# Kernel optimization log

Hardware: AMD Instinct MI355X
Metric: run time of the kernel (lower is better)

Reference implementation:

```python
import jax, jax.numpy as jnp
import numpy as np

B, N, IN_DIM = 2, 2048, 1024
DIM, DEPTH, HEADS, DH = 512, 4, 8, 128
INNER = HEADS * DH  # 1024
MLP, NCLS = 1024, 2
EPS = 1e-5


def setup_inputs() -> dict:
    key = jax.random.key(0)
    ks = jax.random.split(key, 10)
    r = lambda k, shape: (jax.random.normal(k, shape, dtype=jnp.float32) * 0.02)
    return {
        "x": jax.random.normal(ks[0], (B, N, IN_DIM), dtype=jnp.float32),
        "mask": jnp.ones((B, N), dtype=jnp.float32),
        "proj_w": r(ks[1], (IN_DIM, DIM)),
        "proj_b": jnp.zeros((DIM,), jnp.float32),
        "cls_token": jax.random.normal(ks[2], (1, 1, DIM), dtype=jnp.float32),
        "ln1_g": jnp.ones((DEPTH, DIM), jnp.float32),
        "ln1_b": jnp.zeros((DEPTH, DIM), jnp.float32),
        "qkv_w": r(ks[3], (DEPTH, DIM, 3 * INNER)),
        "out_w": r(ks[4], (DEPTH, INNER, DIM)),
        "out_b": jnp.zeros((DEPTH, DIM), jnp.float32),
        "ln2_g": jnp.ones((DEPTH, DIM), jnp.float32),
        "ln2_b": jnp.zeros((DEPTH, DIM), jnp.float32),
        "ff_w1": r(ks[5], (DEPTH, DIM, MLP)),
        "ff_b1": jnp.zeros((DEPTH, MLP), jnp.float32),
        "ff_w2": r(ks[6], (DEPTH, MLP, DIM)),
        "ff_b2": jnp.zeros((DEPTH, DIM), jnp.float32),
        "norm_g": jnp.ones((DIM,), jnp.float32),
        "norm_b": jnp.zeros((DIM,), jnp.float32),
        "head_ln_g": jnp.ones((DIM,), jnp.float32),
        "head_ln_b": jnp.zeros((DIM,), jnp.float32),
        "head_w": r(ks[7], (DIM, NCLS)),
        "head_b": jnp.zeros((NCLS,), jnp.float32),
    }


def _ln(x, g, b):
    m = jnp.mean(x, axis=-1, keepdims=True)
    v = jnp.mean((x - m) ** 2, axis=-1, keepdims=True)
    return (x - m) * jax.lax.rsqrt(v + EPS) * g + b


def reference(x, mask, proj_w, proj_b, cls_token, ln1_g, ln1_b, qkv_w, out_w,
              out_b, ln2_g, ln2_b, ff_w1, ff_b1, ff_w2, ff_b2, norm_g, norm_b,
              head_ln_g, head_ln_b, head_w, head_b):
    b = x.shape[0]
    scale = DH ** -0.5
    # input projection + ReLU
    h = jax.nn.relu(x @ proj_w + proj_b)  # [b, n, dim]
    # prepend cls token; extend mask with a 1 for it
    cls = jnp.broadcast_to(cls_token, (b, 1, DIM))
    h = jnp.concatenate([cls, h], axis=1)  # [b, n+1, dim]
    m_full = jnp.concatenate([jnp.ones((b, 1), mask.dtype), mask], axis=1)
    keep = (m_full != 0)[:, None, None, :]  # [b,1,1,n+1]

    for l in range(DEPTH):  # NOTE: original blocks have NO residual connections
        hn = _ln(h, ln1_g[l], ln1_b[l])
        qkv = hn @ qkv_w[l]  # [b, n+1, 3*inner]
        q, k, v = jnp.split(qkv, 3, axis=-1)
        resh = lambda t: t.reshape(b, -1, HEADS, DH).transpose(0, 2, 1, 3)
        q, k, v = resh(q), resh(k), resh(v)  # [b, h, n+1, dh]
        dots = jnp.einsum('bhid,bhjd->bhij', q, k) * scale
        dots = jnp.where(keep, dots, -jnp.inf)
        attn = jax.nn.softmax(dots, axis=-1)
        o = jnp.einsum('bhij,bhjd->bhid', attn, v)
        o = o.transpose(0, 2, 1, 3).reshape(b, -1, INNER)
        h = o @ out_w[l] + out_b[l]  # attention out (no residual)
        hn = _ln(h, ln2_g[l], ln2_b[l])
        h = jax.nn.gelu(hn @ ff_w1[l] + ff_b1[l], approximate=False) @ ff_w2[l] + ff_b2[l]

    pooled = h[:, 0]  # cls pooling
    pooled = _ln(pooled, norm_g, norm_b)
    pooled = _ln(pooled, head_ln_g, head_ln_b)
    return pooled @ head_w + head_b  # [b, num_classes]
```

## Files before the change

### kernel.cpp

```cpp
#include <hip/hip_runtime.h>
#include <hip/hip_bf16.h>
#include <stdint.h>

#define B_      2
#define N_      2048
#define S_      2049
#define SP_     2176
#define MP_     (B_*SP_)
#define IN_DIM_ 1024
#define DIM_    512
#define HEADS_  8
#define DH_     128
#define INNER_  1024
#define MLP_    1024
#define DEPTH_  4
#define NKV_    (SP_/64)
#define NCHUNK_ 4
#define TPC_    9

typedef __bf16 bf16;
typedef __bf16 bf16x4 __attribute__((ext_vector_type(4)));
typedef __bf16 bf16x8 __attribute__((ext_vector_type(8)));
typedef float  f32x4  __attribute__((ext_vector_type(4)));

__device__ __forceinline__ int sw64(int r, int c)  { return r*64  + (c ^ ((r&7)<<3)); }
__device__ __forceinline__ int sw128(int r, int c) { return r*128 + (c ^ ((r&7)<<3)); }
__device__ __forceinline__ int swr64(int r, int c) { return r*64  + (c ^ ((((r&7)^((r>>3)&7)))<<3)); }

__global__ __launch_bounds__(256) void wconv_kernel(const float* __restrict__ src,
                                                    bf16* __restrict__ dst,
                                                    int K, int N)
{
    __shared__ float tile[32][33];
    size_t mo = (size_t)blockIdx.z * K * N;
    int n0 = blockIdx.x * 32, k0 = blockIdx.y * 32;
    int tx = threadIdx.x & 31, ty = threadIdx.x >> 5;
#pragma unroll
    for (int i = 0; i < 32; i += 8)
        tile[ty + i][tx] = src[mo + (size_t)(k0 + ty + i) * N + n0 + tx];
    __syncthreads();
#pragma unroll
    for (int i = 0; i < 32; i += 8)
        dst[mo + (size_t)(n0 + ty + i) * K + k0 + tx] = (bf16)tile[tx][ty + i];
}

__global__ __launch_bounds__(256) void xconv_kernel(const float* __restrict__ x,
                                                    bf16* __restrict__ xb)
{
    int idx = blockIdx.x * 256 + threadIdx.x;
    int row = idx >> 7;
    int c   = (idx & 127) * 8;
    int b = row / SP_, s = row - b * SP_;
    bf16x8 v;
    if (s >= 1 && s <= N_) {
        const float* src = x + (size_t)(b * N_ + s - 1) * IN_DIM_ + c;
#pragma unroll
        for (int i = 0; i < 8; ++i) v[i] = (bf16)src[i];
    } else {
#pragma unroll
        for (int i = 0; i < 8; ++i) v[i] = (bf16)0.f;
    }
    *(bf16x8*)&xb[(size_t)row * IN_DIM_ + c] = v;
}

__global__ __launch_bounds__(256) void mask_kernel(const float* __restrict__ mask,
                                                   float* __restrict__ pb)
{
    int j = blockIdx.x * 256 + threadIdx.x;
    int b = blockIdx.y;
    if (j >= SP_) return;
    float v;
    if (j == 0) v = 0.f;
    else if (j <= N_) v = (mask[(size_t)b * N_ + j - 1] != 0.f) ? 0.f : -1e30f;
    else v = -1e30f;
    pb[(size_t)b * SP_ + j] = v;
}

__global__ void cls_kernel(const float* __restrict__ cls, float* __restrict__ h)
{
    h[(size_t)(blockIdx.x * SP_) * DIM_ + threadIdx.x] = cls[threadIdx.x];
}

__global__ __launch_bounds__(256) void ln_kernel(const float* __restrict__ h,
                                                 const float* __restrict__ g,
                                                 const float* __restrict__ bta,
                                                 bf16* __restrict__ out)
{
    int row  = blockIdx.x * 4 + (threadIdx.x >> 6);
    int lane = threadIdx.x & 63;
    const float* x = h + (size_t)row * DIM_;
    float v[8]; float s = 0.f;
#pragma unroll
    for (int i = 0; i < 8; ++i) { v[i] = x[lane + 64 * i]; s += v[i]; }
#pragma unroll
    for (int o = 32; o; o >>= 1) s += __shfl_xor(s, o);
    float mean = s * (1.f / DIM_);
    float vs = 0.f;
#pragma unroll
    for (int i = 0; i < 8; ++i) { float d = v[i] - mean; vs += d * d; }
#pragma unroll
    for (int o = 32; o; o >>= 1) vs += __shfl_xor(vs, o);
    float rstd = rsqrtf(vs * (1.f / DIM_) + 1e-5f);
    bf16* orow = out + (size_t)row * DIM_;
#pragma unroll
    for (int i = 0; i < 8; ++i)
        orow[lane + 64 * i] = (bf16)((v[i] - mean) * rstd * g[lane + 64 * i] + bta[lane + 64 * i]);
}

template<int BM, int BN, int ACT, int OUTBF>
__global__ __launch_bounds__(256) void gemm_bt(const bf16* __restrict__ A,
                                               const bf16* __restrict__ Bt,
                                               const float* __restrict__ bias,
                                               void* __restrict__ Cp,
                                               int M, int N, int K)
{
    constexpr int MF = (BM == 128) ? 4 : ((BN == 128) ? 4 : 2);
    constexpr int NF = (BM == 128) ? 4 : 2;
    constexpr int AT = BM / 32, BT = BN / 32;
    __shared__ __align__(16) bf16 As[BM * 64];
    __shared__ __align__(16) bf16 Bs[BN * 64];
    const int tid  = threadIdx.x;
    const int wave = tid >> 6, lane = tid & 63;
    const int bm = blockIdx.x * BM, bn = blockIdx.y * BN;
    const int wr = (BM == 128) ? (wave >> 1) * 64 : ((BN == 64) ? (wave >> 1) * 32 : 0);
    const int wc = (BM == 128) ? (wave & 1) * 64 : ((BN == 64) ? (wave & 1) * 32 : wave * 32);
    const int fr = lane & 15, fk = (lane >> 4) * 8;

    f32x4 acc[MF][NF];
#pragma unroll
    for (int m = 0; m < MF; ++m)
#pragma unroll
        for (int n = 0; n < NF; ++n) acc[m][n] = (f32x4){0.f, 0.f, 0.f, 0.f};

    bf16x8 apre[AT], bpre[BT];
    auto ldg = [&](int k0) {
#pragma unroll
        for (int t = 0; t < AT; ++t) {
            int e = (t * 256 + tid) * 8;
            apre[t] = *(const bf16x8*)&A[(size_t)(bm + (e >> 6)) * K + k0 + (e & 63)];
        }
#pragma unroll
        for (int t = 0; t < BT; ++t) {
            int e = (t * 256 + tid) * 8;
            bpre[t] = *(const bf16x8*)&Bt[(size_t)(bn + (e >> 6)) * K + k0 + (e & 63)];
        }
    };

    ldg(0);
    for (int k0 = 0; k0 < K; k0 += 64) {
        __syncthreads();
#pragma unroll
        for (int t = 0; t < AT; ++t) {
            int e = (t * 256 + tid) * 8;
            *(bf16x8*)&As[sw64(e >> 6, e & 63)] = apre[t];
        }
#pragma unroll
        for (int t = 0; t < BT; ++t) {
            int e = (t * 256 + tid) * 8;
            *(bf16x8*)&Bs[sw64(e >> 6, e & 63)] = bpre[t];
        }
        __syncthreads();
        if (k0 + 64 < K) ldg(k0 + 64);
#pragma unroll
        for (int kk = 0; kk < 2; ++kk) {
            bf16x8 af[MF], bb[NF];
#pragma unroll
            for (int m = 0; m < MF; ++m) af[m] = *(const bf16x8*)&As[sw64(wr + m * 16 + fr, kk * 32 + fk)];
#pragma unroll
            for (int n = 0; n < NF; ++n) bb[n] = *(const bf16x8*)&Bs[sw64(wc + n * 16 + fr, kk * 32 + fk)];
#pragma unroll
            for (int m = 0; m < MF; ++m)
#pragma unroll
                for (int n = 0; n < NF; ++n)
                    acc[m][n] = __builtin_amdgcn_mfma_f32_16x16x32_bf16(af[m], bb[n], acc[m][n], 0, 0, 0);
        }
    }

    const int fc = lane & 15, fr4 = (lane >> 4) * 4;
#pragma unroll
    for (int n = 0; n < NF; ++n) {
        int col = bn + wc + n * 16 + fc;
        float bv = bias ? bias[col] : 0.f;
#pragma unroll
        for (int m = 0; m < MF; ++m) {
#pragma unroll
            for (int j = 0; j < 4; ++j) {
                int row = bm + wr + m * 16 + fr4 + j;
                float v = acc[m][n][j] + bv;
                if (ACT == 1) v = fmaxf(v, 0.f);
                if (ACT == 2) v = 0.5f * v * (1.f + erff(v * 0.70710678118654752f));
                if (OUTBF) ((bf16*)Cp)[(size_t)row * N + col] = (bf16)v;
                else       ((float*)Cp)[(size_t)row * N + col] = v;
            }
        }
    }
}

__global__ __launch_bounds__(256) void attn_kernel(const bf16* __restrict__ qkv,
                                                   const float* __restrict__ pb,
                                                   bf16* __restrict__ o0,
                                                   bf16* __restrict__ o1,
                                                   bf16* __restrict__ o2,
                                                   bf16* __restrict__ o3,
                                                   float* __restrict__ mlbuf)
{
    __shared__ __align__(16) bf16 KsPs[64 * 128];
    __shared__ __align__(16) bf16 Vt[128 * 64];
    __shared__ float Msk[64];

    const int bh = blockIdx.x, b = bh >> 3, hh = bh & 7;
    const int q0 = blockIdx.y * 128;
    const int chunk = blockIdx.z;
    const int t0 = chunk * TPC_;
    const int t1 = (t0 + TPC_ < NKV_) ? t0 + TPC_ : NKV_;
    bf16* obuf = (chunk == 0) ? o0 : (chunk == 1) ? o1 : (chunk == 2) ? o2 : o3;

    const int tid = threadIdx.x, wave = tid >> 6, lane = tid & 63;
    const int fc = lane & 15, g = lane >> 4, g8 = g * 8, rr0 = g * 4;
    bf16* Pw = &KsPs[wave * 2048];

    const bf16* qb = qkv + (size_t)(b * SP_) * (3 * INNER_) + hh * DH_;
    const bf16* kb = qb + INNER_;
    const bf16* vb = qb + 2 * INNER_;

    bf16x8 aq[2][4];
#pragma unroll
    for (int m = 0; m < 2; ++m)
#pragma unroll
        for (int kk = 0; kk < 4; ++kk)
            aq[m][kk] = *(const bf16x8*)&qb[(size_t)(q0 + wave * 32 + m * 16 + fc) * (3 * INNER_) + kk * 32 + g8];

    const int srow = tid >> 4;
    const int scol = (tid & 15) * 8;
    bf16x8 kreg[4], vreg[4];
    float mreg;

    f32x4 accO[2][8];
#pragma unroll
    for (int m = 0; m < 2; ++m)
#pragma unroll
        for (int f = 0; f < 8; ++f) accO[m][f] = (f32x4){0.f, 0.f, 0.f, 0.f};
    float mrow[2] = {-3e38f, -3e38f};
    float lrow[2] = {0.f, 0.f};
    const float scale = 0.08838834764831845f;

    auto issue = [&](int kt) {
        int j0 = kt * 64;
#pragma unroll
        for (int t = 0; t < 4; ++t) {
            kreg[t] = *(const bf16x8*)&kb[(size_t)(j0 + t * 16 + srow) * (3 * INNER_) + scol];
            vreg[t] = *(const bf16x8*)&vb[(size_t)(j0 + t * 16 + srow) * (3 * INNER_) + scol];
        }
        mreg = pb[(size_t)b * SP_ + j0 + (tid & 63)];
    };

    issue(t0);
    for (int kt = t0; kt < t1; ++kt) {
        __syncthreads();
        {
#pragma unroll
            for (int t = 0; t < 4; ++t) {
                *(bf16x8*)&KsPs[sw128(t * 16 + srow, scol)] = kreg[t];
#pragma unroll
                for (int i = 0; i < 8; ++i) Vt[swr64(scol + i, t * 16 + srow)] = vreg[t][i];
            }
            if (tid < 64) Msk[tid] = mreg;
        }
        __syncthreads();
        if (kt + 1 < t1) issue(kt + 1);

        f32x4 sf[2][4];
#pragma unroll
        for (int m = 0; m < 2; ++m)
#pragma unroll
            for (int f = 0; f < 4; ++f) sf[m][f] = (f32x4){0.f, 0.f, 0.f, 0.f};
        __builtin_amdgcn_s_setprio(1);
#pragma unroll
        for (int kk = 0; kk < 4; ++kk) {
            bf16x8 bk[4];
#pragma unroll
            for (int f = 0; f < 4; ++f) bk[f] = *(const bf16x8*)&KsPs[sw128(f * 16 + fc, kk * 32 + g8)];
#pragma unroll
            for (int m = 0; m < 2; ++m)
#pragma unroll
                for (int f = 0; f < 4; ++f)
                    sf[m][f] = __builtin_amdgcn_mfma_f32_16x16x32_bf16(bk[f], aq[m][kk], sf[m][f], 0, 0, 0);
        }
        __builtin_amdgcn_s_setprio(0);

        float rmax[2] = {-3e38f, -3e38f};
#pragma unroll
        for (int f = 0; f < 4; ++f) {
            f32x4 mb = *(const f32x4*)&Msk[f * 16 + rr0];
#pragma unroll
            for (int m = 0; m < 2; ++m)
#pragma unroll
                for (int r = 0; r < 4; ++r) {
                    float s = sf[m][f][r] * scale + mb[r];
                    sf[m][f][r] = s;
                    rmax[m] = fmaxf(rmax[m], s);
                }
        }
#pragma unroll
        for (int m = 0; m < 2; ++m) {
            rmax[m] = fmaxf(rmax[m], __shfl_xor(rmax[m], 16));
            rmax[m] = fmaxf(rmax[m], __shfl_xor(rmax[m], 32));
            if (__any(rmax[m] > mrow[m] + 5.f)) {
                float mn = fmaxf(mrow[m], rmax[m]);
                float corr = __expf(mrow[m] - mn);
                mrow[m] = mn;
                lrow[m] *= corr;
                float c0 = __shfl(corr, rr0 + 0);
                float c1 = __shfl(corr, rr0 + 1);
                float c2 = __shfl(corr, rr0 + 2);
                float c3 = __shfl(corr, rr0 + 3);
#pragma unroll
                for (int f = 0; f < 8; ++f) {
                    accO[m][f][0] *= c0; accO[m][f][1] *= c1;
                    accO[m][f][2] *= c2; accO[m][f][3] *= c3;
                }
            }
        }
        bf16x4 pw[2][4];
#pragma unroll
        for (int m = 0; m < 2; ++m)
#pragma unroll
            for (int f = 0; f < 4; ++f) {
#pragma unroll
                for (int r = 0; r < 4; ++r) {
                    float p = __expf(sf[m][f][r] - mrow[m]);
                    lrow[m] += p;
                    pw[m][f][r] = (bf16)p;
                }
            }
        __syncthreads();
#pragma unroll
        for (int m = 0; m < 2; ++m)
#pragma unroll
            for (int f = 0; f < 4; ++f)
                *(bf16x4*)&Pw[swr64(m * 16 + fc, f * 16 + rr0)] = pw[m][f];

        __builtin_amdgcn_s_setprio(1);
#pragma unroll
        for (int kk = 0; kk < 2; ++kk) {
            bf16x8 ap[2];
#pragma unroll
            for (int m = 0; m < 2; ++m) ap[m] = *(const bf16x8*)&Pw[swr64(m * 16 + fc, kk * 32 + g8)];
#pragma unroll
            for (int f = 0; f < 8; ++f) {
                bf16x8 bv = *(const bf16x8*)&Vt[swr64(f * 16 + fc, kk * 32 + g8)];
#pragma unroll
                for (int m = 0; m < 2; ++m)
                    accO[m][f] = __builtin_amdgcn_mfma_f32_16x16x32_bf16(ap[m], bv, accO[m][f], 0, 0, 0);
            }
        }
        __builtin_amdgcn_s_setprio(0);
    }

#pragma unroll
    for (int m = 0; m < 2; ++m) {
        float l = lrow[m];
        l += __shfl_xor(l, 16);
        l += __shfl_xor(l, 32);
        if (g == 0) {
            int q = q0 + wave * 32 + m * 16 + fc;
            size_t mi = ((size_t)(chunk * B_ * HEADS_ + bh) * SP_ + q) * 2;
            mlbuf[mi + 0] = mrow[m];
            mlbuf[mi + 1] = l;
        }
        float linv = (l > 0.f) ? 1.f / l : 0.f;
        float l0 = __shfl(linv, rr0 + 0);
        float l1 = __shfl(linv, rr0 + 1);
        float l2 = __shfl(linv, rr0 + 2);
        float l3 = __shfl(linv, rr0 + 3);
#pragma unroll
        for (int f = 0; f < 8; ++f) {
            int col = hh * DH_ + f * 16 + fc;
            size_t base = (size_t)(b * SP_ + q0 + wave * 32 + m * 16 + rr0) * INNER_ + col;
            obuf[base + 0 * INNER_] = (bf16)(accO[m][f][0] * l0);
            obuf[base + 1 * INNER_] = (bf16)(accO[m][f][1] * l1);
            obuf[base + 2 * INNER_] = (bf16)(accO[m][f][2] * l2);
            obuf[base + 3 * INNER_] = (bf16)(accO[m][f][3] * l3);
        }
    }
}

__global__ __launch_bounds__(256) void attn_combine_kernel(const bf16* __restrict__ o0,
                                                           const bf16* __restrict__ o1,
                                                           const bf16* __restrict__ o2,
                                                           bf16* __restrict__ o3,
                                                           const float* __restrict__ mlbuf)
{
    const int bh = blockIdx.y, b = bh >> 3, hh = bh & 7;
    int gx = blockIdx.x * 256 + threadIdx.x;
    int q  = gx >> 4;
    int d  = (gx & 15) * 8;

    float mv[NCHUNK_], lv[NCHUNK_];
#pragma unroll
    for (int c = 0; c < NCHUNK_; ++c) {
        size_t mi = ((size_t)(c * B_ * HEADS_ + bh) * SP_ + q) * 2;
        mv[c] = mlbuf[mi];
        lv[c] = mlbuf[mi + 1];
    }
    float M = mv[0];
#pragma unroll
    for (int c = 1; c < NCHUNK_; ++c) M = fmaxf(M, mv[c]);
    float w[NCHUNK_], den = 0.f;
#pragma unroll
    for (int c = 0; c < NCHUNK_; ++c) { w[c] = lv[c] * __expf(mv[c] - M); den += w[c]; }
    float r = (den > 0.f) ? 1.f / den : 0.f;

    size_t base = (size_t)(b * SP_ + q) * INNER_ + hh * DH_ + d;
    bf16x8 v0 = *(const bf16x8*)&o0[base];
    bf16x8 v1 = *(const bf16x8*)&o1[base];
    bf16x8 v2 = *(const bf16x8*)&o2[base];
    bf16x8 v3 = *(const bf16x8*)&o3[base];
    bf16x8 out;
#pragma unroll
    for (int i = 0; i < 8; ++i)
        out[i] = (bf16)((w[0] * (float)v0[i] + w[1] * (float)v1[i]
                       + w[2] * (float)v2[i] + w[3] * (float)v3[i]) * r);
    *(bf16x8*)&o3[base] = out;
}

__global__ __launch_bounds__(64) void head_kernel(const float* __restrict__ h,
                                                  const float* __restrict__ ng, const float* __restrict__ nb,
                                                  const float* __restrict__ hg, const float* __restrict__ hb,
                                                  const float* __restrict__ hw, const float* __restrict__ hbi,
                                                  float* __restrict__ out)
{
    int b = blockIdx.x, lane = threadIdx.x;
    const float* xr = h + (size_t)(b * SP_) * DIM_;
    float v[8]; float s = 0.f;
#pragma unroll
    for (int i = 0; i < 8; ++i) { v[i] = xr[lane + 64 * i]; s += v[i]; }
#pragma unroll
    for (int o = 32; o; o >>= 1) s += __shfl_xor(s, o);
    float mean = s * (1.f / DIM_); float vs = 0.f;
#pragma unroll
    for (int i = 0; i < 8; ++i) { float d = v[i] - mean; vs += d * d; }
#pragma unroll
    for (int o = 32; o; o >>= 1) vs += __shfl_xor(vs, o);
    float rstd = rsqrtf(vs * (1.f / DIM_) + 1e-5f);
#pragma unroll
    for (int i = 0; i < 8; ++i) v[i] = (v[i] - mean) * rstd * ng[lane + 64 * i] + nb[lane + 64 * i];
    s = 0.f;
#pragma unroll
    for (int i = 0; i < 8; ++i) s += v[i];
#pragma unroll
    for (int o = 32; o; o >>= 1) s += __shfl_xor(s, o);
    mean = s * (1.f / DIM_); vs = 0.f;
#pragma unroll
    for (int i = 0; i < 8; ++i) { float d = v[i] - mean; vs += d * d; }
#pragma unroll
    for (int o = 32; o; o >>= 1) vs += __shfl_xor(vs, o);
    rstd = rsqrtf(vs * (1.f / DIM_) + 1e-5f);
#pragma unroll
    for (int i = 0; i < 8; ++i) v[i] = (v[i] - mean) * rstd * hg[lane + 64 * i] + hb[lane + 64 * i];
    float a0 = 0.f, a1 = 0.f;
#pragma unroll
    for (int i = 0; i < 8; ++i) {
        a0 += v[i] * hw[(lane + 64 * i) * 2 + 0];
        a1 += v[i] * hw[(lane + 64 * i) * 2 + 1];
    }
#pragma unroll
    for (int o = 32; o; o >>= 1) { a0 += __shfl_xor(a0, o); a1 += __shfl_xor(a1, o); }
    if (lane == 0) { out[b * 2 + 0] = a0 + hbi[0]; out[b * 2 + 1] = a1 + hbi[1]; }
}

extern "C" void kernel_launch(void* const* d_in, const int* in_sizes, int n_in,
                              void* d_out, int out_size, void* d_ws, size_t ws_size,
                              hipStream_t stream)
{
    const float* x       = (const float*)d_in[0];
    const float* mask    = (const float*)d_in[1];
    const float* proj_w  = (const float*)d_in[2];
    const float* proj_b  = (const float*)d_in[3];
    const float* cls_tok = (const float*)d_in[4];
    const float* ln1_g   = (const float*)d_in[5];
    const float* ln1_b   = (const float*)d_in[6];
    const float* qkv_w   = (const float*)d_in[7];
    const float* out_w   = (const float*)d_in[8];
    const float* out_b   = (const float*)d_in[9];
    const float* ln2_g   = (const float*)d_in[10];
    const float* ln2_b   = (const float*)d_in[11];
    const float* ff_w1   = (const float*)d_in[12];
    const float* ff_b1   = (const float*)d_in[13];
    const float* ff_w2   = (const float*)d_in[14];
    const float* ff_b2   = (const float*)d_in[15];
    const float* norm_g  = (const float*)d_in[16];
    const float* norm_b  = (const float*)d_in[17];
    const float* hln_g   = (const float*)d_in[18];
    const float* hln_b   = (const float*)d_in[19];
    const float* head_w  = (const float*)d_in[20];
    const float* head_b  = (const float*)d_in[21];

    char* p = (char*)d_ws;
    auto alloc = [&](size_t bytes) { char* r = p; p += (bytes + 255) & ~(size_t)255; return r; };
    bf16*  x_bf    = (bf16*)alloc((size_t)MP_ * IN_DIM_ * 2);
    float* h       = (float*)alloc((size_t)MP_ * DIM_ * 4);
    bf16*  hn_bf   = (bf16*)alloc((size_t)MP_ * DIM_ * 2);
    bf16*  qkv_bf  = (bf16*)alloc((size_t)MP_ * 3 * INNER_ * 2);
    bf16*  o_bf    = (bf16*)alloc((size_t)MP_ * INNER_ * 2);
    bf16*  ff1_bf  = (bf16*)alloc((size_t)MP_ * MLP_ * 2);
    bf16*  proj_wt = (bf16*)alloc((size_t)DIM_ * IN_DIM_ * 2);
    bf16*  qkv_wt  = (bf16*)alloc((size_t)DEPTH_ * 3 * INNER_ * DIM_ * 2);
    bf16*  out_wt  = (bf16*)alloc((size_t)DEPTH_ * DIM_ * INNER_ * 2);
    bf16*  ff1_wt  = (bf16*)alloc((size_t)DEPTH_ * MLP_ * DIM_ * 2);
    bf16*  ff2_wt  = (bf16*)alloc((size_t)DEPTH_ * DIM_ * MLP_ * 2);
    float* pbias   = (float*)alloc((size_t)B_ * SP_ * 4);
    if ((size_t)(p - (char*)d_ws) > ws_size) return;
    float* mlbuf = (float*)hn_bf;

    wconv_kernel<<<dim3(DIM_ / 32, IN_DIM_ / 32, 1), 256, 0, stream>>>(proj_w, proj_wt, IN_DIM_, DIM_);
    wconv_kernel<<<dim3(3 * INNER_ / 32, DIM_ / 32, DEPTH_), 256, 0, stream>>>(qkv_w, qkv_wt, DIM_, 3 * INNER_);
    wconv_kernel<<<dim3(DIM_ / 32, INNER_ / 32, DEPTH_), 256, 0, stream>>>(out_w, out_wt, INNER_, DIM_);
    wconv_kernel<<<dim3(MLP_ / 32, DIM_ / 32, DEPTH_), 256, 0, stream>>>(ff_w1, ff1_wt, DIM_, MLP_);
    wconv_kernel<<<dim3(DIM_ / 32, MLP_ / 32, DEPTH_), 256, 0, stream>>>(ff_w2, ff2_wt, MLP_, DIM_);

    xconv_kernel<<<MP_ * IN_DIM_ / 8 / 256, 256, 0, stream>>>(x, x_bf);
    mask_kernel<<<dim3((SP_ + 255) / 256, B_), 256, 0, stream>>>(mask, pbias);

    gemm_bt<64, 64, 1, 0><<<dim3(MP_ / 64, DIM_ / 64), 256, 0, stream>>>(x_bf, proj_wt, proj_b, h, MP_, DIM_, IN_DIM_);
    cls_kernel<<<B_, DIM_, 0, stream>>>(cls_tok, h);

    for (int l = 0; l < DEPTH_; ++l) {
        ln_kernel<<<MP_ / 4, 256, 0, stream>>>(h, ln1_g + l * DIM_, ln1_b + l * DIM_, hn_bf);
        gemm_bt<128, 128, 0, 1><<<dim3(MP_ / 128, 3 * INNER_ / 128), 256, 0, stream>>>(
            hn_bf, qkv_wt + (size_t)l * 3 * INNER_ * DIM_, nullptr, qkv_bf, MP_, 3 * INNER_, DIM_);
        attn_kernel<<<dim3(B_ * HEADS_, SP_ / 128, NCHUNK_), 256, 0, stream>>>(
            qkv_bf, pbias, x_bf, ff1_bf, (bf16*)h, o_bf, mlbuf);
        attn_combine_kernel<<<dim3(SP_ * 16 / 256, B_ * HEADS_), 256, 0, stream>>>(
            x_bf, ff1_bf, (const bf16*)h, o_bf, mlbuf);
        gemm_bt<64, 64, 0, 0><<<dim3(MP_ / 64, DIM_ / 64), 256, 0, stream>>>(
            o_bf, out_wt + (size_t)l * DIM_ * INNER_, out_b + l * DIM_, h, MP_, DIM_, INNER_);
        ln_kernel<<<MP_ / 4, 256, 0, stream>>>(h, ln2_g + l * DIM_, ln2_b + l * DIM_, hn_bf);
        gemm_bt<64, 128, 2, 1><<<dim3(MP_ / 64, MLP_ / 128), 256, 0, stream>>>(
            hn_bf, ff1_wt + (size_t)l * MLP_ * DIM_, ff_b1 + l * MLP_, ff1_bf, MP_, MLP_, DIM_);
        gemm_bt<64, 64, 0, 0><<<dim3(MP_ / 64, DIM_ / 64), 256, 0, stream>>>(
            ff1_bf, ff2_wt + (size_t)l * DIM_ * MLP_, ff_b2 + l * DIM_, h, MP_, DIM_, MLP_);
    }

    head_kernel<<<B_, 64, 0, stream>>>(h, norm_g, norm_b, hln_g, hln_b, head_w, head_b, (float*)d_out);
}
```

Measured before the change: 816.7 us.

## Use direct global-to-LDS loads in GEMM and attention, pre-transpose V

Result: slower. 1.105 ms (+35.3%).

```diff
diff --git a/kernel.cpp b/kernel.cpp
--- a/kernel.cpp
+++ b/kernel.cpp
@@ -23,9 +23,11 @@
 typedef __bf16 bf16x8 __attribute__((ext_vector_type(8)));
 typedef float  f32x4  __attribute__((ext_vector_type(4)));
 
-__device__ __forceinline__ int sw64(int r, int c)  { return r*64  + (c ^ ((r&7)<<3)); }
-__device__ __forceinline__ int sw128(int r, int c) { return r*128 + (c ^ ((r&7)<<3)); }
-__device__ __forceinline__ int swr64(int r, int c) { return r*64  + (c ^ ((((r&7)^((r>>3)&7)))<<3)); }
+#define AS1 __attribute__((address_space(1)))
+#define AS3 __attribute__((address_space(3)))
+__device__ __forceinline__ void gload16(const bf16* g, bf16* l) {
+    __builtin_amdgcn_global_load_lds((const AS1 void*)g, (AS3 void*)l, 16, 0, 0);
+}
 
 __global__ __launch_bounds__(256) void wconv_kernel(const float* __restrict__ src,
                                                     bf16* __restrict__ dst,
@@ -79,6 +81,30 @@
 __global__ void cls_kernel(const float* __restrict__ cls, float* __restrict__ h)
 {
     h[(size_t)(blockIdx.x * SP_) * DIM_ + threadIdx.x] = cls[threadIdx.x];
+}
+
+__global__ __launch_bounds__(256) void vt_kernel(const bf16* __restrict__ qkv,
+                                                 bf16* __restrict__ vT)
+{
+    __shared__ __align__(16) bf16 tile[64][72];
+    const int bh = blockIdx.z, b = bh >> 3, hh = bh & 7;
+    const int j0 = blockIdx.x * 64, d0 = blockIdx.y * 64;
+    const int t = threadIdx.x;
+    const int jr = t >> 3, dc = (t & 7) * 8;
+    const bf16* src = qkv + (size_t)(b * SP_) * (3 * INNER_) + 2 * INNER_ + hh * DH_ + d0;
+#pragma unroll
+    for (int h2 = 0; h2 < 2; ++h2) {
+        bf16x8 v = *(const bf16x8*)&src[(size_t)(j0 + jr + h2 * 32) * (3 * INNER_) + dc];
+#pragma unroll
+        for (int i = 0; i < 8; ++i) tile[dc + i][jr + h2 * 32] = v[i];
+    }
+    __syncthreads();
+#pragma unroll
+    for (int h2 = 0; h2 < 2; ++h2) {
+        int dr = (t >> 3) + h2 * 32;
+        int jc = (t & 7) * 8;
+        *(bf16x8*)&vT[((size_t)bh * DH_ + d0 + dr) * SP_ + j0 + jc] = *(const bf16x8*)&tile[dr][jc];
+    }
 }
 
 __global__ __launch_bounds__(256) void ln_kernel(const float* __restrict__ h,
@@ -125,6 +151,7 @@
     const int wr = (BM == 128) ? (wave >> 1) * 64 : ((BN == 64) ? (wave >> 1) * 32 : 0);
     const int wc = (BM == 128) ? (wave & 1) * 64 : ((BN == 64) ? (wave & 1) * 32 : wave * 32);
     const int fr = lane & 15, fk = (lane >> 4) * 8;
+    const int gr = lane >> 3, gc = (lane & 7) * 8;
 
     f32x4 acc[MF][NF];
 #pragma unroll
@@ -132,48 +159,40 @@
 #pragma unroll
         for (int n = 0; n < NF; ++n) acc[m][n] = (f32x4){0.f, 0.f, 0.f, 0.f};
 
-    bf16x8 apre[AT], bpre[BT];
-    auto ldg = [&](int k0) {
+    for (int k0 = 0; k0 < K; k0 += 64) {
 #pragma unroll
         for (int t = 0; t < AT; ++t) {
-            int e = (t * 256 + tid) * 8;
-            apre[t] = *(const bf16x8*)&A[(size_t)(bm + (e >> 6)) * K + k0 + (e & 63)];
+            int chunk = wave * AT + t;
+            int r = chunk * 8 + gr;
+            gload16(&A[(size_t)(bm + r) * K + k0 + (gc ^ ((r & 7) << 3))], &As[chunk * 512]);
         }
 #pragma unroll
         for (int t = 0; t < BT; ++t) {
-            int e = (t * 256 + tid) * 8;
-            bpre[t] = *(const bf16x8*)&Bt[(size_t)(bn + (e >> 6)) * K + k0 + (e & 63)];
-        }
-    };
-
-    ldg(0);
-    for (int k0 = 0; k0 < K; k0 += 64) {
+            int chunk = wave * BT + t;
+            int r = chunk * 8 + gr;
+            gload16(&Bt[(size_t)(bn + r) * K + k0 + (gc ^ ((r & 7) << 3))], &Bs[chunk * 512]);
+        }
         __syncthreads();
-#pragma unroll
-        for (int t = 0; t < AT; ++t) {
-            int e = (t * 256 + tid) * 8;
-            *(bf16x8*)&As[sw64(e >> 6, e & 63)] = apre[t];
-        }
-#pragma unroll
-        for (int t = 0; t < BT; ++t) {
-            int e = (t * 256 + tid) * 8;
-            *(bf16x8*)&Bs[sw64(e >> 6, e & 63)] = bpre[t];
-        }
-        __syncthreads();
-        if (k0 + 64 < K) ldg(k0 + 64);
 #pragma unroll
         for (int kk = 0; kk < 2; ++kk) {
             bf16x8 af[MF], bb[NF];
 #pragma unroll
-            for (int m = 0; m < MF; ++m) af[m] = *(const bf16x8*)&As[sw64(wr + m * 16 + fr, kk * 32 + fk)];
-#pragma unroll
-            for (int n = 0; n < NF; ++n) bb[n] = *(const bf16x8*)&Bs[sw64(wc + n * 16 + fr, kk * 32 + fk)];
+            for (int m = 0; m < MF; ++m) {
+                int r = wr + m * 16 + fr;
+                af[m] = *(const bf16x8*)&As[r * 64 + ((kk * 32 + fk) ^ ((r & 7) << 3))];
+            }
+#pragma unroll
+            for (int n = 0; n < NF; ++n) {
+                int r = wc + n * 16 + fr;
+                bb[n] = *(const bf16x8*)&Bs[r * 64 + ((kk * 32 + fk) ^ ((r & 7) << 3))];
+            }
 #pragma unroll
             for (int m = 0; m < MF; ++m)
 #pragma unroll
                 for (int n = 0; n < NF; ++n)
                     acc[m][n] = __builtin_amdgcn_mfma_f32_16x16x32_bf16(af[m], bb[n], acc[m][n], 0, 0, 0);
         }
+        __syncthreads();
     }
 
     const int fc = lane & 15, fr4 = (lane >> 4) * 4;
@@ -196,17 +215,18 @@
     }
 }
 
-__global__ __launch_bounds__(256) void attn_kernel(const bf16* __restrict__ qkv,
-                                                   const float* __restrict__ pb,
-                                                   bf16* __restrict__ o0,
-                                                   bf16* __restrict__ o1,
-                                                   bf16* __restrict__ o2,
-                                                   bf16* __restrict__ o3,
-                                                   float* __restrict__ mlbuf)
-{
-    __shared__ __align__(16) bf16 KsPs[64 * 128];
+__global__ __launch_bounds__(256, 3) void attn_kernel(const bf16* __restrict__ qkv,
+                                                      const bf16* __restrict__ vT,
+                                                      const float* __restrict__ pb,
+                                                      bf16* __restrict__ o0,
+                                                      bf16* __restrict__ o1,
+                                                      bf16* __restrict__ o2,
+                                                      bf16* __restrict__ o3,
+                                                      float* __restrict__ mlbuf)
+{
+    __shared__ __align__(16) bf16 Ks[64 * 128];
     __shared__ __align__(16) bf16 Vt[128 * 64];
-    __shared__ float Msk[64];
+    __shared__ __align__(16) bf16 Ps[4][32 * 64];
 
     const int bh = blockIdx.x, b = bh >> 3, hh = bh & 7;
     const int q0 = blockIdx.y * 128;
@@ -217,11 +237,12 @@
 
     const int tid = threadIdx.x, wave = tid >> 6, lane = tid & 63;
     const int fc = lane & 15, g = lane >> 4, g8 = g * 8, rr0 = g * 4;
-    bf16* Pw = &KsPs[wave * 2048];
-
-    const bf16* qb = qkv + (size_t)(b * SP_) * (3 * INNER_) + hh * DH_;
-    const bf16* kb = qb + INNER_;
-    const bf16* vb = qb + 2 * INNER_;
+    bf16* Pw = &Ps[wave][0];
+
+    const bf16* qb  = qkv + (size_t)(b * SP_) * (3 * INNER_) + hh * DH_;
+    const bf16* kb  = qb + INNER_;
+    const bf16* vTb = vT + (size_t)bh * DH_ * SP_;
+    const float* pbb = pb + (size_t)b * SP_;
 
     bf16x8 aq[2][4];
 #pragma unroll
@@ -230,10 +251,7 @@
         for (int kk = 0; kk < 4; ++kk)
             aq[m][kk] = *(const bf16x8*)&qb[(size_t)(q0 + wave * 32 + m * 16 + fc) * (3 * INNER_) + kk * 32 + g8];
 
-    const int srow = tid >> 4;
-    const int scol = (tid & 15) * 8;
-    bf16x8 kreg[4], vreg[4];
-    float mreg;
+    bf16x8 vreg[4];
 
     f32x4 accO[2][8];
 #pragma unroll
@@ -244,30 +262,38 @@
     float lrow[2] = {0.f, 0.f};
     const float scale = 0.08838834764831845f;
 
-    auto issue = [&](int kt) {
+    auto issueK = [&](int kt) {
         int j0 = kt * 64;
 #pragma unroll
         for (int t = 0; t < 4; ++t) {
-            kreg[t] = *(const bf16x8*)&kb[(size_t)(j0 + t * 16 + srow) * (3 * INNER_) + scol];
-            vreg[t] = *(const bf16x8*)&vb[(size_t)(j0 + t * 16 + srow) * (3 * INNER_) + scol];
-        }
-        mreg = pb[(size_t)b * SP_ + j0 + (tid & 63)];
+            int ck = wave * 4 + t;
+            int r = ck * 4 + (lane >> 4);
+            int cp = (lane & 15) * 8;
+            gload16(&kb[(size_t)(j0 + r) * (3 * INNER_) + (cp ^ ((r & 15) << 3))], &Ks[ck * 512]);
+        }
     };
-
-    issue(t0);
+    auto issueV = [&](int kt) {
+        int j0 = kt * 64;
+#pragma unroll
+        for (int i = 0; i < 4; ++i) {
+            int idx = i * 256 + tid;
+            int d = idx >> 3, jp = (idx & 7) * 8;
+            vreg[i] = *(const bf16x8*)&vTb[(size_t)d * SP_ + j0 + (jp ^ ((d & 7) << 3))];
+        }
+    };
+
+    issueV(t0);
+    issueK(t0);
     for (int kt = t0; kt < t1; ++kt) {
+        int j0 = kt * 64;
         __syncthreads();
-        {
-#pragma unroll
-            for (int t = 0; t < 4; ++t) {
-                *(bf16x8*)&KsPs[sw128(t * 16 + srow, scol)] = kreg[t];
-#pragma unroll
-                for (int i = 0; i < 8; ++i) Vt[swr64(scol + i, t * 16 + srow)] = vreg[t][i];
-            }
-            if (tid < 64) Msk[tid] = mreg;
+#pragma unroll
+        for (int i = 0; i < 4; ++i) {
+            int idx = i * 256 + tid;
+            *(bf16x8*)&Vt[idx * 8] = vreg[i];
         }
         __syncthreads();
-        if (kt + 1 < t1) issue(kt + 1);
+        if (kt + 1 < t1) issueV(kt + 1);
 
         f32x4 sf[2][4];
 #pragma unroll
@@ -279,7 +305,10 @@
         for (int kk = 0; kk < 4; ++kk) {
             bf16x8 bk[4];
 #pragma unroll
-            for (int f = 0; f < 4; ++f) bk[f] = *(const bf16x8*)&KsPs[sw128(f * 16 + fc, kk * 32 + g8)];
+            for (int f = 0; f < 4; ++f) {
+                int r = f * 16 + fc;
+                bk[f] = *(const bf16x8*)&Ks[r * 128 + ((kk * 32 + g8) ^ ((r & 15) << 3))];
+            }
 #pragma unroll
             for (int m = 0; m < 2; ++m)
 #pragma unroll
@@ -287,11 +316,13 @@
                     sf[m][f] = __builtin_amdgcn_mfma_f32_16x16x32_bf16(bk[f], aq[m][kk], sf[m][f], 0, 0, 0);
         }
         __builtin_amdgcn_s_setprio(0);
+        __syncthreads();
+        if (kt + 1 < t1) issueK(kt + 1);
 
         float rmax[2] = {-3e38f, -3e38f};
 #pragma unroll
         for (int f = 0; f < 4; ++f) {
-            f32x4 mb = *(const f32x4*)&Msk[f * 16 + rr0];
+            f32x4 mb = *(const f32x4*)&pbb[j0 + f * 16 + rr0];
 #pragma unroll
             for (int m = 0; m < 2; ++m)
 #pragma unroll
@@ -321,34 +352,33 @@
                 }
             }
         }
-        bf16x4 pw[2][4];
 #pragma unroll
         for (int m = 0; m < 2; ++m)
 #pragma unroll
             for (int f = 0; f < 4; ++f) {
+                bf16x4 pw;
 #pragma unroll
                 for (int r = 0; r < 4; ++r) {
                     float p = __expf(sf[m][f][r] - mrow[m]);
                     lrow[m] += p;
-                    pw[m][f][r] = (bf16)p;
+                    pw[r] = (bf16)p;
                 }
-            }
-        __syncthreads();
-#pragma unroll
-        for (int m = 0; m < 2; ++m)
-#pragma unroll
-            for (int f = 0; f < 4; ++f)
-                *(bf16x4*)&Pw[swr64(m * 16 + fc, f * 16 + rr0)] = pw[m][f];
-
+                int rq = m * 16 + fc;
+                *(bf16x4*)&Pw[rq * 64 + ((f * 16 + rr0) ^ ((rq & 7) << 3))] = pw;
+            }
         __builtin_amdgcn_s_setprio(1);
 #pragma unroll
         for (int kk = 0; kk < 2; ++kk) {
             bf16x8 ap[2];
 #pragma unroll
-            for (int m = 0; m < 2; ++m) ap[m] = *(const bf16x8*)&Pw[swr64(m * 16 + fc, kk * 32 + g8)];
+            for (int m = 0; m < 2; ++m) {
+                int rq = m * 16 + fc;
+                ap[m] = *(const bf16x8*)&Pw[rq * 64 + ((kk * 32 + g8) ^ ((rq & 7) << 3))];
+            }
 #pragma unroll
             for (int f = 0; f < 8; ++f) {
-                bf16x8 bv = *(const bf16x8*)&Vt[swr64(f * 16 + fc, kk * 32 + g8)];
+                int rd = f * 16 + fc;
+                bf16x8 bv = *(const bf16x8*)&Vt[rd * 64 + ((kk * 32 + g8) ^ ((rd & 7) << 3))];
 #pragma unroll
                 for (int m = 0; m < 2; ++m)
                     accO[m][f] = __builtin_amdgcn_mfma_f32_16x16x32_bf16(ap[m], bv, accO[m][f], 0, 0, 0);
@@ -504,6 +534,7 @@
     bf16*  qkv_bf  = (bf16*)alloc((size_t)MP_ * 3 * INNER_ * 2);
     bf16*  o_bf    = (bf16*)alloc((size_t)MP_ * INNER_ * 2);
     bf16*  ff1_bf  = (bf16*)alloc((size_t)MP_ * MLP_ * 2);
+    bf16*  vT      = (bf16*)alloc((size_t)B_ * HEADS_ * DH_ * SP_ * 2);
     bf16*  proj_wt = (bf16*)alloc((size_t)DIM_ * IN_DIM_ * 2);
     bf16*  qkv_wt  = (bf16*)alloc((size_t)DEPTH_ * 3 * INNER_ * DIM_ * 2);
     bf16*  out_wt  = (bf16*)alloc((size_t)DEPTH_ * DIM_ * INNER_ * 2);
@@ -529,8 +560,9 @@
         ln_kernel<<<MP_ / 4, 256, 0, stream>>>(h, ln1_g + l * DIM_, ln1_b + l * DIM_, hn_bf);
         gemm_bt<128, 128, 0, 1><<<dim3(MP_ / 128, 3 * INNER_ / 128), 256, 0, stream>>>(
             hn_bf, qkv_wt + (size_t)l * 3 * INNER_ * DIM_, nullptr, qkv_bf, MP_, 3 * INNER_, DIM_);
+        vt_kernel<<<dim3(SP_ / 64, DH_ / 64, B_ * HEADS_), 256, 0, stream>>>(qkv_bf, vT);
         attn_kernel<<<dim3(B_ * HEADS_, SP_ / 128, NCHUNK_), 256, 0, stream>>>(
-            qkv_bf, pbias, x_bf, ff1_bf, (bf16*)h, o_bf, mlbuf);
+            qkv_bf, vT, pbias, x_bf, ff1_bf, (bf16*)h, o_bf, mlbuf);
         attn_combine_kernel<<<dim3(SP_ * 16 / 256, B_ * HEADS_), 256, 0, stream>>>(
             x_bf, ff1_bf, (const bf16*)h, o_bf, mlbuf);
         gemm_bt<64, 64, 0, 0><<<dim3(MP_ / 64, DIM_ / 64), 256, 0, stream>>>(
```
